# Kernel optimization log

Hardware: AMD Instinct MI355X
Metric: run time of the kernel (lower is better)

Reference implementation:

```python
import jax, jax.numpy as jnp
import numpy as np

B, N, FH, H, FO = 8, 1024, 128, 8, 64
FIN = 2 * FH  # f_hid * 2
NEG = -1e9
SLOPE = 0.2  # leaky_relu negative slope (GAT default)


def setup_inputs() -> dict:
    key = jax.random.key(0)
    ks = jax.random.split(key, 10)
    x = jax.random.normal(ks[0], (B, FIN), jnp.float32)
    A = jax.random.randint(ks[1], (B, N, N), 0, 2, jnp.int32)  # 0/1 dense adjacency
    mask_zero = jnp.ones((B, N, 1), jnp.float32)  # node validity mask
    p_atten = jax.random.uniform(ks[2], (B, N), jnp.float32)  # unused in forward body
    e_atten = jax.random.uniform(ks[3], (B, N, FIN), jnp.float32)
    Npost = jax.random.normal(ks[4], (N, FIN), jnp.float32) * np.float32(1.0 / np.sqrt(FIN))  # kaiming-ish
    w = jax.random.normal(ks[5], (H, FIN, FO), jnp.float32) * np.float32(1.0 / np.sqrt(FIN))
    a_src = jax.random.normal(ks[6], (H, FO), jnp.float32) * np.float32(0.1)
    a_dst = jax.random.normal(ks[7], (H, FO), jnp.float32) * np.float32(0.1)
    bias = jnp.zeros((FO,), jnp.float32)
    return {"x": x, "A": A, "mask_zero": mask_zero, "p_atten": p_atten,
            "e_atten": e_atten, "Npost": Npost, "w": w, "a_src": a_src,
            "a_dst": a_dst, "bias": bias}


def reference(x, A, mask_zero, p_atten, e_atten, Npost, w, a_src, a_dst, bias):
    # broadcast-mul feature gating: x [B,FIN] repeated over N posts, gated by Npost*e_atten
    recx = x[:, None, :] * (Npost[None, :, :] * e_atten)          # [B,N,FIN]
    # BatchGAT (DeepInf-style multi-head graph attention, dropout disabled / eval mode)
    h = jnp.einsum('bnf,hfo->bhno', recx, w)                      # [B,H,N,FO]
    s = jnp.einsum('bhno,ho->bhn', h, a_src)                      # src attention term
    d = jnp.einsum('bhno,ho->bhn', h, a_dst)                      # dst attention term
    logits = jax.nn.leaky_relu(s[:, :, :, None] + d[:, :, None, :], SLOPE)  # [B,H,N,N]
    adj = (A > 0)[:, None, :, :]                                  # [B,1,N,N]
    logits = jnp.where(adj, logits, NEG)
    attn = jax.nn.softmax(logits, axis=-1)                        # masked row softmax
    out = jnp.einsum('bhnm,bhmo->bhno', attn, h) + bias           # aggregate neighbors
    out = out.mean(axis=1)                                        # average heads -> [B,N,FO]
    return out * mask_zero                                        # zero padded nodes
```

## Files before the change

### kernel.cpp

```cpp
#include <hip/hip_runtime.h>

typedef __attribute__((ext_vector_type(8))) short          bf16x8;
typedef __attribute__((ext_vector_type(8))) unsigned short u16x8;
typedef __attribute__((ext_vector_type(4))) unsigned short u16x4;
typedef __attribute__((ext_vector_type(4))) float          f32x4;
typedef __attribute__((ext_vector_type(4))) unsigned int   u32x4;

union U8 { u16x8 u; bf16x8 b; u32x4 w; };
union U4 { u16x4 u; unsigned w[2]; };

__device__ __forceinline__ unsigned short f2bf(float f){
  unsigned u = __float_as_uint(f);
  return (unsigned short)((u + 0x7fffu + ((u >> 16) & 1u)) >> 16);
}
__device__ __forceinline__ unsigned pack_bf16(float lo, float hi){
  unsigned a = __float_as_uint(hi) + 0x8000u;
  unsigned b = __float_as_uint(lo) + 0x8000u;
  return __builtin_amdgcn_perm(a, b, 0x07060302u);
}
__device__ __forceinline__ unsigned maskpack(float e0, float e1, unsigned m){
  unsigned r;
  asm("v_cvt_pk_bf16_f32 %0, %1, %2" : "=v"(r) : "v"(e0), "v"(e1));
  return r & m;
}

#define NN  1024
#define FIN 256
#define NH  8
#define FO  64

__global__ __launch_bounds__(256) void stage0(
    const float* __restrict__ w, const int* __restrict__ A,
    const float* __restrict__ bias, const float* __restrict__ mz,
    unsigned short* __restrict__ wfrag, unsigned* __restrict__ emask,
    float* __restrict__ out)
{
  const int tid = blockIdx.x * 256 + threadIdx.x;
  if (tid < 16384){
    const int lane = tid & 63, ss = (tid >> 6) & 3, kc = (tid >> 8) & 7, h = tid >> 11;
    const int o = 16 * ss + (lane & 15);
    const int f = kc * 32 + (lane >> 4) * 8;
    u16x8 r;
    #pragma unroll
    for (int j = 0; j < 8; j++) r[j] = f2bf(w[(h * FIN + f + j) * FO + o]);
    *(u16x8*)(wfrag + tid * 8) = r;
  }
  #pragma unroll
  for (int k = 0; k < 2; k++){
    const int i = tid + k * 262144;
    out[i] = bias[i & 63] * mz[i >> 6];
  }
  const int4* A4 = (const int4*)A;
  for (int i = tid; i < 1048576; i += 262144){
    const int4 a0 = A4[2 * i], a1 = A4[2 * i + 1];
    u32x4 m;
    m[0] = (a0.x > 0 ? 0xFFFFu : 0u) | (a0.y > 0 ? 0xFFFF0000u : 0u);
    m[1] = (a0.z > 0 ? 0xFFFFu : 0u) | (a0.w > 0 ? 0xFFFF0000u : 0u);
    m[2] = (a1.x > 0 ? 0xFFFFu : 0u) | (a1.y > 0 ? 0xFFFF0000u : 0u);
    m[3] = (a1.z > 0 ? 0xFFFFu : 0u) | (a1.w > 0 ? 0xFFFF0000u : 0u);
    *(u32x4*)(emask + 4 * i) = m;
  }
}

__global__ __launch_bounds__(512, 4) void stageA(
    const float* __restrict__ x, const float* __restrict__ e_at,
    const float* __restrict__ Np, const unsigned short* __restrict__ wfrag,
    const float* __restrict__ a_src, const float* __restrict__ a_dst,
    unsigned short* __restrict__ hT,
    float* __restrict__ Rt, float* __restrict__ expd, float* __restrict__ expd2)
{
  __shared__ unsigned short rex[16 * 264];
  const int t = threadIdx.x;
  const int n0 = blockIdx.x * 16, b = blockIdx.y;

  {
    const int row = t >> 5, f0 = (t & 31) * 8;
    const int nrow = n0 + row;
    const float* ep = e_at + (b * NN + nrow) * FIN + f0;
    const float* qp = Np + nrow * FIN + f0;
    const float* xp = x + b * FIN + f0;
    f32x4 e0 = *(const f32x4*)ep, e1 = *(const f32x4*)(ep + 4);
    f32x4 q0 = *(const f32x4*)qp, q1 = *(const f32x4*)(qp + 4);
    f32x4 x0 = *(const f32x4*)xp, x1 = *(const f32x4*)(xp + 4);
    u16x8 r;
    #pragma unroll
    for (int j = 0; j < 4; j++){
      r[j]     = f2bf(e0[j] * q0[j] * x0[j]);
      r[j + 4] = f2bf(e1[j] * q1[j] * x1[j]);
    }
    *(u16x8*)(rex + row * 264 + f0) = r;
  }
  __syncthreads();

  const int h = t >> 6, lane = t & 63, quad = lane >> 4, l15 = lane & 15;
  const unsigned short* wf = wfrag + h * 16384 + lane * 8;

  f32x4 acc[4] = {};
  #pragma unroll
  for (int kc = 0; kc < 8; kc++){
    U8 a0, bf[4];
    a0.u = *(const u16x8*)(rex + l15 * 264 + kc * 32 + quad * 8);
    #pragma unroll
    for (int ss = 0; ss < 4; ss++) bf[ss].u = *(const u16x8*)(wf + (kc * 4 + ss) * 512);
    #pragma unroll
    for (int ss = 0; ss < 4; ss++)
      acc[ss] = __builtin_amdgcn_mfma_f32_16x16x32_bf16(a0.b, bf[ss].b, acc[ss], 0, 0, 0);
  }

  {
    const int mtile = blockIdx.x >> 1, moff = (blockIdx.x & 1) * 16;
    unsigned short* pan = hT + (size_t)(((b * NH + h) * 32 + mtile) * 64) * 32;
    #pragma unroll
    for (int ss = 0; ss < 4; ss++){
      U4 v;
      v.w[0] = pack_bf16(acc[ss][0], acc[ss][1]);
      v.w[1] = pack_bf16(acc[ss][2], acc[ss][3]);
      *(u16x4*)(pan + (16 * ss + l15) * 32 + moff + quad * 4) = v.u;
    }
  }

  float as4[4], ad4[4];
  #pragma unroll
  for (int ss = 0; ss < 4; ss++){
    as4[ss] = a_src[h * FO + 16 * ss + l15];
    ad4[ss] = a_dst[h * FO + 16 * ss + l15];
  }
  #pragma unroll
  for (int i = 0; i < 4; i++){
    float ps = 0.f, pd = 0.f;
    #pragma unroll
    for (int ss = 0; ss < 4; ss++){ ps += acc[ss][i] * as4[ss]; pd += acc[ss][i] * ad4[ss]; }
    #pragma unroll
    for (int off = 1; off < 16; off <<= 1){
      ps += __shfl_xor(ps, off);
      pd += __shfl_xor(pd, off);
    }
    if (l15 == 0){
      const int idx = (b * NH + h) * NN + n0 + quad * 4 + i;
      Rt[idx]    = __expf(0.8f * ps);
      expd[idx]  = __expf(pd);
      expd2[idx] = __expf(0.2f * pd);
    }
  }
}

__global__ __launch_bounds__(512, 8) void stageB(
    const unsigned* __restrict__ emask,
    const unsigned short* __restrict__ hT,
    const float* __restrict__ Rt,
    const float* __restrict__ expd, const float* __restrict__ expd2,
    const float* __restrict__ mz, float* __restrict__ out)
{
  __shared__ float ed_l[2 * NN];
  __shared__ float e2_l[2 * NN];
  __shared__ float l_l[4 * 16];
  const int t = threadIdx.x;
  const int n0 = blockIdx.x * 32, hq = blockIdx.y, b = blockIdx.z;
  const int w = t >> 6, lane = t & 63, quad = lane >> 4, l15 = lane & 15;
  const int hl = w & 1, rg = (w >> 1) & 1, mh = w >> 2;
  const int h = hq * 2 + hl;

  if (t < 64) l_l[t] = 0.f;
  {
    const float* s1 = expd  + (b * NH + hq * 2) * NN;
    const float* s2 = expd2 + (b * NH + hq * 2) * NN;
    *(f32x4*)(ed_l + t * 4) = *(const f32x4*)(s1 + t * 4);
    *(f32x4*)(e2_l + t * 4) = *(const f32x4*)(s2 + t * 4);
  }
  __syncthreads();

  const int row = n0 + rg * 16 + l15;
  const float Rv = Rt[(b * NH + h) * NN + row];
  const unsigned short* pb = hT + (size_t)(b * NH + h) * 65536 + l15 * 32 + quad * 8;
  const float* edh = ed_l + hl * NN + quad * 8;
  const float* e2h = e2_l + hl * NN + quad * 8;
  const unsigned* emp = emask + ((size_t)(b * NN) + row) * 512 + quad * 4;
  const int c0 = mh * 16;

  U8 pan[4];
  #pragma unroll
  for (int ss = 0; ss < 4; ss++)
    pan[ss].u = *(const u16x8*)(pb + (size_t)c0 * 2048 + ss * 512);
  u32x4 em = *(const u32x4*)(emp + c0 * 16);

  U8 ones;
  #pragma unroll
  for (int j = 0; j < 8; j++) ones.u[j] = 0x3F80;

  f32x4 acc[4] = {};
  f32x4 accl = {};

  for (int cc = 0; cc < 16; cc++){
    const int c = c0 + cc;
    f32x4 d01 = *(const f32x4*)(edh + c * 32);
    f32x4 d23 = *(const f32x4*)(edh + c * 32 + 4);
    f32x4 g01 = *(const f32x4*)(e2h + c * 32);
    f32x4 g23 = *(const f32x4*)(e2h + c * 32 + 4);
    f32x4 p01 = Rv * d01, p23 = Rv * d23;
    U8 p;
    p.w[0] = maskpack(fmaxf(p01[0], g01[0]), fmaxf(p01[1], g01[1]), em[0]);
    p.w[1] = maskpack(fmaxf(p01[2], g01[2]), fmaxf(p01[3], g01[3]), em[1]);
    p.w[2] = maskpack(fmaxf(p23[0], g23[0]), fmaxf(p23[1], g23[1]), em[2]);
    p.w[3] = maskpack(fmaxf(p23[2], g23[2]), fmaxf(p23[3], g23[3]), em[3]);
    #pragma unroll
    for (int ss = 0; ss < 4; ss++)
      acc[ss] = __builtin_amdgcn_mfma_f32_16x16x32_bf16(p.b, pan[ss].b, acc[ss], 0, 0, 0);
    accl = __builtin_amdgcn_mfma_f32_16x16x32_bf16(p.b, ones.b, accl, 0, 0, 0);
    if (cc + 1 < 16){
      #pragma unroll
      for (int ss = 0; ss < 4; ss++)
        pan[ss].u = *(const u16x8*)(pb + (size_t)(c + 1) * 2048 + ss * 512);
      em = *(const u32x4*)(emp + (c + 1) * 16);
    }
  }

  if (l15 == 0){
    #pragma unroll
    for (int i = 0; i < 4; i++)
      atomicAdd(&l_l[(w & 3) * 16 + quad * 4 + i], accl[i]);
  }
  __syncthreads();

  const float* mzp = mz + b * NN + n0 + rg * 16;
  #pragma unroll
  for (int i = 0; i < 4; i++){
    const int r = quad * 4 + i;
    const float invm = (0.125f / l_l[(w & 3) * 16 + r]) * mzp[r];
    float* op = out + (size_t)(b * NN + n0 + rg * 16 + r) * FO + l15;
    #pragma unroll
    for (int ss = 0; ss < 4; ss++)
      atomicAdd(op + ss * 16, acc[ss][i] * invm);
  }
}

extern "C" void kernel_launch(void* const* d_in, const int* in_sizes, int n_in,
                              void* d_out, int out_size, void* d_ws, size_t ws_size,
                              hipStream_t stream)
{
  (void)in_sizes; (void)n_in; (void)out_size; (void)ws_size;
  const float* x    = (const float*)d_in[0];
  const int*   A    = (const int*)d_in[1];
  const float* mz   = (const float*)d_in[2];
  const float* e_at = (const float*)d_in[4];
  const float* Np   = (const float*)d_in[5];
  const float* w    = (const float*)d_in[6];
  const float* asrc = (const float*)d_in[7];
  const float* adst = (const float*)d_in[8];
  const float* bias = (const float*)d_in[9];
  float* out = (float*)d_out;

  char* ws = (char*)d_ws;
  unsigned short* wfrag = (unsigned short*)ws;
  unsigned short* hT    = (unsigned short*)(ws + 262144);
  float* Rt    = (float*)(ws + 8650752);
  float* expd  = (float*)(ws + 8912896);
  float* expd2 = (float*)(ws + 9175040);
  unsigned* emask = (unsigned*)(ws + 9437184);

  stage0<<<dim3(1024), dim3(256), 0, stream>>>(w, A, bias, mz, wfrag, emask, out);
  stageA<<<dim3(64, 8), dim3(512), 0, stream>>>(x, e_at, Np, wfrag, asrc, adst,
                                                hT, Rt, expd, expd2);
  stageB<<<dim3(32, 4, 8), dim3(512), 0, stream>>>(emask, hT, Rt, expd, expd2,
                                                   mz, out);
}
```

Before: 178.7 us.

## Pack adjacency into bitmask and have each stageB wave process two row groups

stage0 now compresses the int adjacency into a 1-bit-per-edge mask with wave ballots, replacing the 16-bit-per-edge mask. This shrinks the mask written to the workspace and read back by stageB by a factor of 16. stageB loads its 32 rows of bits into LDS and expands them through a 16-entry lookup table. Each wave now computes both 16-row groups, so every hT panel fragment loaded from global memory feeds twice as many MFMAs. The launch becomes 256-thread blocks on a 1D grid with a remapped block order. The cost is more registers per thread, extra LDS lookups, and fewer waves per block.

```diff
diff --git a/kernel.cpp b/kernel.cpp
--- a/kernel.cpp
+++ b/kernel.cpp
@@ -32,7 +32,7 @@
 __global__ __launch_bounds__(256) void stage0(
     const float* __restrict__ w, const int* __restrict__ A,
     const float* __restrict__ bias, const float* __restrict__ mz,
-    unsigned short* __restrict__ wfrag, unsigned* __restrict__ emask,
+    unsigned short* __restrict__ wfrag, unsigned long long* __restrict__ Abits,
     float* __restrict__ out)
 {
   const int tid = blockIdx.x * 256 + threadIdx.x;
@@ -50,15 +50,9 @@
     const int i = tid + k * 262144;
     out[i] = bias[i & 63] * mz[i >> 6];
   }
-  const int4* A4 = (const int4*)A;
-  for (int i = tid; i < 1048576; i += 262144){
-    const int4 a0 = A4[2 * i], a1 = A4[2 * i + 1];
-    u32x4 m;
-    m[0] = (a0.x > 0 ? 0xFFFFu : 0u) | (a0.y > 0 ? 0xFFFF0000u : 0u);
-    m[1] = (a0.z > 0 ? 0xFFFFu : 0u) | (a0.w > 0 ? 0xFFFF0000u : 0u);
-    m[2] = (a1.x > 0 ? 0xFFFFu : 0u) | (a1.y > 0 ? 0xFFFF0000u : 0u);
-    m[3] = (a1.z > 0 ? 0xFFFFu : 0u) | (a1.w > 0 ? 0xFFFF0000u : 0u);
-    *(u32x4*)(emask + 4 * i) = m;
+  for (int i = tid; i < 8388608; i += 262144){
+    unsigned long long m = __ballot(A[i] > 0);
+    if ((threadIdx.x & 63) == 0) Abits[i >> 6] = m;
   }
 }
 
@@ -144,8 +138,8 @@
   }
 }
 
-__global__ __launch_bounds__(512, 8) void stageB(
-    const unsigned* __restrict__ emask,
+__global__ __launch_bounds__(256, 4) void stageB(
+    const unsigned* __restrict__ Aw,
     const unsigned short* __restrict__ hT,
     const float* __restrict__ Rt,
     const float* __restrict__ expd, const float* __restrict__ expd2,
@@ -153,83 +147,131 @@
 {
   __shared__ float ed_l[2 * NN];
   __shared__ float e2_l[2 * NN];
+  __shared__ unsigned mask_l[32 * 33];
+  __shared__ __align__(8) unsigned lut[16][2];
   __shared__ float l_l[4 * 16];
+
+  const int fid = blockIdx.x;
+  const int gb = (fid & 7) * 128 + (fid >> 3);
+  const int n0 = (gb & 31) * 32, hq = (gb >> 5) & 3, b = gb >> 7;
+
   const int t = threadIdx.x;
-  const int n0 = blockIdx.x * 32, hq = blockIdx.y, b = blockIdx.z;
   const int w = t >> 6, lane = t & 63, quad = lane >> 4, l15 = lane & 15;
-  const int hl = w & 1, rg = (w >> 1) & 1, mh = w >> 2;
+  const int hl = w & 1, mh = w >> 1;
   const int h = hq * 2 + hl;
 
   if (t < 64) l_l[t] = 0.f;
+  if (t < 16){
+    lut[t][0] = (t & 1 ? 0xFFFFu : 0u) | (t & 2 ? 0xFFFF0000u : 0u);
+    lut[t][1] = (t & 4 ? 0xFFFFu : 0u) | (t & 8 ? 0xFFFF0000u : 0u);
+  }
   {
     const float* s1 = expd  + (b * NH + hq * 2) * NN;
     const float* s2 = expd2 + (b * NH + hq * 2) * NN;
-    *(f32x4*)(ed_l + t * 4) = *(const f32x4*)(s1 + t * 4);
-    *(f32x4*)(e2_l + t * 4) = *(const f32x4*)(s2 + t * 4);
+    *(f32x4*)(ed_l + t * 8)     = *(const f32x4*)(s1 + t * 8);
+    *(f32x4*)(ed_l + t * 8 + 4) = *(const f32x4*)(s1 + t * 8 + 4);
+    *(f32x4*)(e2_l + t * 8)     = *(const f32x4*)(s2 + t * 8);
+    *(f32x4*)(e2_l + t * 8 + 4) = *(const f32x4*)(s2 + t * 8 + 4);
+  }
+  #pragma unroll
+  for (int k = 0; k < 4; k++){
+    const int i = t + k * 256;
+    mask_l[(i >> 5) * 33 + (i & 31)] = Aw[(b * NN + n0 + (i >> 5)) * 32 + (i & 31)];
   }
   __syncthreads();
 
-  const int row = n0 + rg * 16 + l15;
-  const float Rv = Rt[(b * NH + h) * NN + row];
+  const int hb = (b * NH + h) * NN;
+  const float Rv0 = Rt[hb + n0 + l15];
+  const float Rv1 = Rt[hb + n0 + 16 + l15];
   const unsigned short* pb = hT + (size_t)(b * NH + h) * 65536 + l15 * 32 + quad * 8;
   const float* edh = ed_l + hl * NN + quad * 8;
   const float* e2h = e2_l + hl * NN + quad * 8;
-  const unsigned* emp = emask + ((size_t)(b * NN) + row) * 512 + quad * 4;
   const int c0 = mh * 16;
+  const int qs = quad * 8;
 
   U8 pan[4];
   #pragma unroll
   for (int ss = 0; ss < 4; ss++)
     pan[ss].u = *(const u16x8*)(pb + (size_t)c0 * 2048 + ss * 512);
-  u32x4 em = *(const u32x4*)(emp + c0 * 16);
+  unsigned mw0 = mask_l[l15 * 33 + c0];
+  unsigned mw1 = mask_l[(16 + l15) * 33 + c0];
 
   U8 ones;
   #pragma unroll
   for (int j = 0; j < 8; j++) ones.u[j] = 0x3F80;
 
-  f32x4 acc[4] = {};
-  f32x4 accl = {};
+  f32x4 acc0[4] = {}, acc1[4] = {};
+  f32x4 accl0 = {}, accl1 = {};
 
   for (int cc = 0; cc < 16; cc++){
     const int c = c0 + cc;
-    f32x4 d01 = *(const f32x4*)(edh + c * 32);
-    f32x4 d23 = *(const f32x4*)(edh + c * 32 + 4);
-    f32x4 g01 = *(const f32x4*)(e2h + c * 32);
-    f32x4 g23 = *(const f32x4*)(e2h + c * 32 + 4);
-    f32x4 p01 = Rv * d01, p23 = Rv * d23;
-    U8 p;
-    p.w[0] = maskpack(fmaxf(p01[0], g01[0]), fmaxf(p01[1], g01[1]), em[0]);
-    p.w[1] = maskpack(fmaxf(p01[2], g01[2]), fmaxf(p01[3], g01[3]), em[1]);
-    p.w[2] = maskpack(fmaxf(p23[0], g23[0]), fmaxf(p23[1], g23[1]), em[2]);
-    p.w[3] = maskpack(fmaxf(p23[2], g23[2]), fmaxf(p23[3], g23[3]), em[3]);
-    #pragma unroll
-    for (int ss = 0; ss < 4; ss++)
-      acc[ss] = __builtin_amdgcn_mfma_f32_16x16x32_bf16(p.b, pan[ss].b, acc[ss], 0, 0, 0);
-    accl = __builtin_amdgcn_mfma_f32_16x16x32_bf16(p.b, ones.b, accl, 0, 0, 0);
+    const unsigned am0 = (mw0 >> qs) & 0xFF;
+    const unsigned am1 = (mw1 >> qs) & 0xFF;
+    const uint2 la0 = *(const uint2*)&lut[am0 & 15][0];
+    const uint2 lb0 = *(const uint2*)&lut[(am0 >> 4) & 15][0];
+    const uint2 la1 = *(const uint2*)&lut[am1 & 15][0];
+    const uint2 lb1 = *(const uint2*)&lut[(am1 >> 4) & 15][0];
+    if (cc + 1 < 16){
+      mw0 = mask_l[l15 * 33 + c + 1];
+      mw1 = mask_l[(16 + l15) * 33 + c + 1];
+    }
+    const f32x4 d01 = *(const f32x4*)(edh + c * 32);
+    const f32x4 d23 = *(const f32x4*)(edh + c * 32 + 4);
+    const f32x4 g01 = *(const f32x4*)(e2h + c * 32);
+    const f32x4 g23 = *(const f32x4*)(e2h + c * 32 + 4);
+    {
+      const f32x4 p01 = Rv0 * d01, p23 = Rv0 * d23;
+      U8 p;
+      p.w[0] = maskpack(fmaxf(p01[0], g01[0]), fmaxf(p01[1], g01[1]), la0.x);
+      p.w[1] = maskpack(fmaxf(p01[2], g01[2]), fmaxf(p01[3], g01[3]), la0.y);
+      p.w[2] = maskpack(fmaxf(p23[0], g23[0]), fmaxf(p23[1], g23[1]), lb0.x);
+      p.w[3] = maskpack(fmaxf(p23[2], g23[2]), fmaxf(p23[3], g23[3]), lb0.y);
+      #pragma unroll
+      for (int ss = 0; ss < 4; ss++)
+        acc0[ss] = __builtin_amdgcn_mfma_f32_16x16x32_bf16(p.b, pan[ss].b, acc0[ss], 0, 0, 0);
+      accl0 = __builtin_amdgcn_mfma_f32_16x16x32_bf16(p.b, ones.b, accl0, 0, 0, 0);
+    }
+    {
+      const f32x4 p01 = Rv1 * d01, p23 = Rv1 * d23;
+      U8 p;
+      p.w[0] = maskpack(fmaxf(p01[0], g01[0]), fmaxf(p01[1], g01[1]), la1.x);
+      p.w[1] = maskpack(fmaxf(p01[2], g01[2]), fmaxf(p01[3], g01[3]), la1.y);
+      p.w[2] = maskpack(fmaxf(p23[0], g23[0]), fmaxf(p23[1], g23[1]), lb1.x);
+      p.w[3] = maskpack(fmaxf(p23[2], g23[2]), fmaxf(p23[3], g23[3]), lb1.y);
+      #pragma unroll
+      for (int ss = 0; ss < 4; ss++)
+        acc1[ss] = __builtin_amdgcn_mfma_f32_16x16x32_bf16(p.b, pan[ss].b, acc1[ss], 0, 0, 0);
+      accl1 = __builtin_amdgcn_mfma_f32_16x16x32_bf16(p.b, ones.b, accl1, 0, 0, 0);
+    }
     if (cc + 1 < 16){
       #pragma unroll
       for (int ss = 0; ss < 4; ss++)
         pan[ss].u = *(const u16x8*)(pb + (size_t)(c + 1) * 2048 + ss * 512);
-      em = *(const u32x4*)(emp + (c + 1) * 16);
     }
   }
 
   if (l15 == 0){
     #pragma unroll
-    for (int i = 0; i < 4; i++)
-      atomicAdd(&l_l[(w & 3) * 16 + quad * 4 + i], accl[i]);
+    for (int i = 0; i < 4; i++){
+      atomicAdd(&l_l[(hl * 2 + 0) * 16 + quad * 4 + i], accl0[i]);
+      atomicAdd(&l_l[(hl * 2 + 1) * 16 + quad * 4 + i], accl1[i]);
+    }
   }
   __syncthreads();
 
-  const float* mzp = mz + b * NN + n0 + rg * 16;
+  const float* mzp = mz + b * NN + n0;
   #pragma unroll
   for (int i = 0; i < 4; i++){
-    const int r = quad * 4 + i;
-    const float invm = (0.125f / l_l[(w & 3) * 16 + r]) * mzp[r];
-    float* op = out + (size_t)(b * NN + n0 + rg * 16 + r) * FO + l15;
-    #pragma unroll
-    for (int ss = 0; ss < 4; ss++)
-      atomicAdd(op + ss * 16, acc[ss][i] * invm);
+    const int r16 = quad * 4 + i;
+    const float invm0 = (0.125f / l_l[(hl * 2 + 0) * 16 + r16]) * mzp[r16];
+    const float invm1 = (0.125f / l_l[(hl * 2 + 1) * 16 + r16]) * mzp[16 + r16];
+    float* op0 = out + (size_t)(b * NN + n0 + r16) * FO + l15;
+    float* op1 = out + (size_t)(b * NN + n0 + 16 + r16) * FO + l15;
+    #pragma unroll
+    for (int ss = 0; ss < 4; ss++){
+      atomicAdd(op0 + ss * 16, acc0[ss][i] * invm0);
+      atomicAdd(op1 + ss * 16, acc1[ss][i] * invm1);
+    }
   }
 }
 
@@ -255,11 +297,11 @@
   float* Rt    = (float*)(ws + 8650752);
   float* expd  = (float*)(ws + 8912896);
   float* expd2 = (float*)(ws + 9175040);
-  unsigned* emask = (unsigned*)(ws + 9437184);
-
-  stage0<<<dim3(1024), dim3(256), 0, stream>>>(w, A, bias, mz, wfrag, emask, out);
+  unsigned long long* Abits = (unsigned long long*)(ws + 9437184);
+
+  stage0<<<dim3(1024), dim3(256), 0, stream>>>(w, A, bias, mz, wfrag, Abits, out);
   stageA<<<dim3(64, 8), dim3(512), 0, stream>>>(x, e_at, Np, wfrag, asrc, adst,
                                                 hT, Rt, expd, expd2);
-  stageB<<<dim3(32, 4, 8), dim3(512), 0, stream>>>(emask, hT, Rt, expd, expd2,
-                                                   mz, out);
-}
+  stageB<<<dim3(1024), dim3(256), 0, stream>>>((const unsigned*)Abits, hT,
+                                               Rt, expd, expd2, mz, out);
+}
```

Result: faster. 158.0 us (-11.6%).

## Pack adjacency into bitmask in stageA and reduce heads in LDS without atomics

Applied to the files above, without the earlier changes.

The adjacency conversion moves from stage0 into stageA. It now writes 1 bit per edge using wave ballots instead of a 16-bit mask per edge, which shrinks the mask the attention kernel has to read by a large factor. The attention kernel is restructured so that one block handles all 8 heads for a 16-row tile. Head averaging, bias and the node mask are applied through an LDS reduction, replacing global float atomics and the separate output init. Each wave now walks the full 1024 columns with double-buffered panel loads. This cuts parallelism per block and adds bit-expansion ALU work in the inner loop.

```diff
diff --git a/kernel.cpp b/kernel.cpp
--- a/kernel.cpp
+++ b/kernel.cpp
@@ -23,6 +23,11 @@
   asm("v_cvt_pk_bf16_f32 %0, %1, %2" : "=v"(r) : "v"(e0), "v"(e1));
   return r & m;
 }
+__device__ __forceinline__ unsigned bit2half(unsigned m, unsigned off){
+  unsigned lo = __builtin_amdgcn_sbfe((int)m, off, 1u);
+  unsigned hi = __builtin_amdgcn_sbfe((int)m, off + 1u, 1u);
+  return __builtin_amdgcn_perm(hi, lo, 0x05040100u);
+}
 
 #define NN  1024
 #define FIN 256
@@ -30,48 +35,31 @@
 #define FO  64
 
 __global__ __launch_bounds__(256) void stage0(
-    const float* __restrict__ w, const int* __restrict__ A,
-    const float* __restrict__ bias, const float* __restrict__ mz,
-    unsigned short* __restrict__ wfrag, unsigned* __restrict__ emask,
-    float* __restrict__ out)
+    const float* __restrict__ w, unsigned short* __restrict__ wfrag)
 {
   const int tid = blockIdx.x * 256 + threadIdx.x;
-  if (tid < 16384){
-    const int lane = tid & 63, ss = (tid >> 6) & 3, kc = (tid >> 8) & 7, h = tid >> 11;
-    const int o = 16 * ss + (lane & 15);
-    const int f = kc * 32 + (lane >> 4) * 8;
-    u16x8 r;
-    #pragma unroll
-    for (int j = 0; j < 8; j++) r[j] = f2bf(w[(h * FIN + f + j) * FO + o]);
-    *(u16x8*)(wfrag + tid * 8) = r;
-  }
-  #pragma unroll
-  for (int k = 0; k < 2; k++){
-    const int i = tid + k * 262144;
-    out[i] = bias[i & 63] * mz[i >> 6];
-  }
-  const int4* A4 = (const int4*)A;
-  for (int i = tid; i < 1048576; i += 262144){
-    const int4 a0 = A4[2 * i], a1 = A4[2 * i + 1];
-    u32x4 m;
-    m[0] = (a0.x > 0 ? 0xFFFFu : 0u) | (a0.y > 0 ? 0xFFFF0000u : 0u);
-    m[1] = (a0.z > 0 ? 0xFFFFu : 0u) | (a0.w > 0 ? 0xFFFF0000u : 0u);
-    m[2] = (a1.x > 0 ? 0xFFFFu : 0u) | (a1.y > 0 ? 0xFFFF0000u : 0u);
-    m[3] = (a1.z > 0 ? 0xFFFFu : 0u) | (a1.w > 0 ? 0xFFFF0000u : 0u);
-    *(u32x4*)(emask + 4 * i) = m;
-  }
+  const int lane = tid & 63, ss = (tid >> 6) & 3, kc = (tid >> 8) & 7, h = tid >> 11;
+  const int o = 16 * ss + (lane & 15);
+  const int f = kc * 32 + (lane >> 4) * 8;
+  u16x8 r;
+  #pragma unroll
+  for (int j = 0; j < 8; j++) r[j] = f2bf(w[(h * FIN + f + j) * FO + o]);
+  *(u16x8*)(wfrag + tid * 8) = r;
 }
 
 __global__ __launch_bounds__(512, 4) void stageA(
     const float* __restrict__ x, const float* __restrict__ e_at,
     const float* __restrict__ Np, const unsigned short* __restrict__ wfrag,
     const float* __restrict__ a_src, const float* __restrict__ a_dst,
+    const int* __restrict__ A, unsigned long long* __restrict__ Abits,
     unsigned short* __restrict__ hT,
     float* __restrict__ Rt, float* __restrict__ expd, float* __restrict__ expd2)
 {
   __shared__ unsigned short rex[16 * 264];
   const int t = threadIdx.x;
-  const int n0 = blockIdx.x * 16, b = blockIdx.y;
+  const int fid = blockIdx.x;
+  const int b = fid & 7, tile = fid >> 3;
+  const int n0 = tile * 16;
 
   {
     const int row = t >> 5, f0 = (t & 31) * 8;
@@ -108,7 +96,7 @@
   }
 
   {
-    const int mtile = blockIdx.x >> 1, moff = (blockIdx.x & 1) * 16;
+    const int mtile = tile >> 1, moff = (tile & 1) * 16;
     unsigned short* pan = hT + (size_t)(((b * NH + h) * 32 + mtile) * 64) * 32;
     #pragma unroll
     for (int ss = 0; ss < 4; ss++){
@@ -142,46 +130,56 @@
       expd2[idx] = __expf(0.2f * pd);
     }
   }
-}
-
-__global__ __launch_bounds__(512, 8) void stageB(
-    const unsigned* __restrict__ emask,
+
+  {
+    const int seg = b * 1048576 + tile * 16384;
+    #pragma unroll 4
+    for (int k = 0; k < 32; k++){
+      const int i = seg + k * 512 + t;
+      unsigned long long m = __ballot(A[i] > 0);
+      if ((t & 63) == 0) Abits[i >> 6] = m;
+    }
+  }
+}
+
+__global__ __launch_bounds__(512, 4) void attnBC(
+    const unsigned* __restrict__ Aw,
     const unsigned short* __restrict__ hT,
     const float* __restrict__ Rt,
     const float* __restrict__ expd, const float* __restrict__ expd2,
-    const float* __restrict__ mz, float* __restrict__ out)
-{
-  __shared__ float ed_l[2 * NN];
-  __shared__ float e2_l[2 * NN];
-  __shared__ float l_l[4 * 16];
+    const float* __restrict__ bias, const float* __restrict__ mz,
+    float* __restrict__ out)
+{
+  __shared__ float smem[16384];
+
+  const int fid = blockIdx.x;
+  const int b = fid & 7, rt = fid >> 3;
+  const int n0 = rt * 16;
+
   const int t = threadIdx.x;
-  const int n0 = blockIdx.x * 32, hq = blockIdx.y, b = blockIdx.z;
-  const int w = t >> 6, lane = t & 63, quad = lane >> 4, l15 = lane & 15;
-  const int hl = w & 1, rg = (w >> 1) & 1, mh = w >> 2;
-  const int h = hq * 2 + hl;
-
-  if (t < 64) l_l[t] = 0.f;
-  {
-    const float* s1 = expd  + (b * NH + hq * 2) * NN;
-    const float* s2 = expd2 + (b * NH + hq * 2) * NN;
-    *(f32x4*)(ed_l + t * 4) = *(const f32x4*)(s1 + t * 4);
-    *(f32x4*)(e2_l + t * 4) = *(const f32x4*)(s2 + t * 4);
-  }
-  __syncthreads();
-
-  const int row = n0 + rg * 16 + l15;
-  const float Rv = Rt[(b * NH + h) * NN + row];
+  const int h = t >> 6, lane = t & 63, quad = lane >> 4, l15 = lane & 15;
+
+  #pragma unroll
+  for (int k = 0; k < 4; k++){
+    *(f32x4*)(smem + k * 2048 + t * 4) =
+        *(const f32x4*)(expd + b * 8192 + k * 2048 + t * 4);
+    *(f32x4*)(smem + 8192 + k * 2048 + t * 4) =
+        *(const f32x4*)(expd2 + b * 8192 + k * 2048 + t * 4);
+  }
+  __syncthreads();
+
+  const float Rv = Rt[(b * NH + h) * NN + n0 + l15];
   const unsigned short* pb = hT + (size_t)(b * NH + h) * 65536 + l15 * 32 + quad * 8;
-  const float* edh = ed_l + hl * NN + quad * 8;
-  const float* e2h = e2_l + hl * NN + quad * 8;
-  const unsigned* emp = emask + ((size_t)(b * NN) + row) * 512 + quad * 4;
-  const int c0 = mh * 16;
-
-  U8 pan[4];
+  const float* edh = smem + h * 1024 + quad * 8;
+  const float* e2h = smem + 8192 + h * 1024 + quad * 8;
+  const unsigned* awp = Aw + (b * NN + n0) * 32;
+  const unsigned qs = (unsigned)(quad * 8);
+
+  U8 panc[4], pann[4];
   #pragma unroll
   for (int ss = 0; ss < 4; ss++)
-    pan[ss].u = *(const u16x8*)(pb + (size_t)c0 * 2048 + ss * 512);
-  u32x4 em = *(const u32x4*)(emp + c0 * 16);
+    panc[ss].u = *(const u16x8*)(pb + ss * 512);
+  unsigned mwc = awp[l15 * 32], mwn;
 
   U8 ones;
   #pragma unroll
@@ -190,46 +188,58 @@
   f32x4 acc[4] = {};
   f32x4 accl = {};
 
-  for (int cc = 0; cc < 16; cc++){
-    const int c = c0 + cc;
-    f32x4 d01 = *(const f32x4*)(edh + c * 32);
-    f32x4 d23 = *(const f32x4*)(edh + c * 32 + 4);
-    f32x4 g01 = *(const f32x4*)(e2h + c * 32);
-    f32x4 g23 = *(const f32x4*)(e2h + c * 32 + 4);
-    f32x4 p01 = Rv * d01, p23 = Rv * d23;
-    U8 p;
-    p.w[0] = maskpack(fmaxf(p01[0], g01[0]), fmaxf(p01[1], g01[1]), em[0]);
-    p.w[1] = maskpack(fmaxf(p01[2], g01[2]), fmaxf(p01[3], g01[3]), em[1]);
-    p.w[2] = maskpack(fmaxf(p23[0], g23[0]), fmaxf(p23[1], g23[1]), em[2]);
-    p.w[3] = maskpack(fmaxf(p23[2], g23[2]), fmaxf(p23[3], g23[3]), em[3]);
-    #pragma unroll
-    for (int ss = 0; ss < 4; ss++)
-      acc[ss] = __builtin_amdgcn_mfma_f32_16x16x32_bf16(p.b, pan[ss].b, acc[ss], 0, 0, 0);
-    accl = __builtin_amdgcn_mfma_f32_16x16x32_bf16(p.b, ones.b, accl, 0, 0, 0);
-    if (cc + 1 < 16){
+  #pragma unroll
+  for (int c = 0; c < 32; c++){
+    if (c + 1 < 32){
       #pragma unroll
       for (int ss = 0; ss < 4; ss++)
-        pan[ss].u = *(const u16x8*)(pb + (size_t)(c + 1) * 2048 + ss * 512);
-      em = *(const u32x4*)(emp + (c + 1) * 16);
-    }
-  }
-
-  if (l15 == 0){
-    #pragma unroll
-    for (int i = 0; i < 4; i++)
-      atomicAdd(&l_l[(w & 3) * 16 + quad * 4 + i], accl[i]);
-  }
-  __syncthreads();
-
-  const float* mzp = mz + b * NN + n0 + rg * 16;
+        pann[ss].u = *(const u16x8*)(pb + (size_t)(c + 1) * 2048 + ss * 512);
+      mwn = awp[l15 * 32 + c + 1];
+    }
+    const unsigned lax = bit2half(mwc, qs + 0u), lay = bit2half(mwc, qs + 2u);
+    const unsigned lbx = bit2half(mwc, qs + 4u), lby = bit2half(mwc, qs + 6u);
+    const f32x4 d01 = *(const f32x4*)(edh + c * 32);
+    const f32x4 d23 = *(const f32x4*)(edh + c * 32 + 4);
+    const f32x4 g01 = *(const f32x4*)(e2h + c * 32);
+    const f32x4 g23 = *(const f32x4*)(e2h + c * 32 + 4);
+    const f32x4 p01 = Rv * d01, p23 = Rv * d23;
+    U8 p;
+    p.w[0] = maskpack(fmaxf(p01[0], g01[0]), fmaxf(p01[1], g01[1]), lax);
+    p.w[1] = maskpack(fmaxf(p01[2], g01[2]), fmaxf(p01[3], g01[3]), lay);
+    p.w[2] = maskpack(fmaxf(p23[0], g23[0]), fmaxf(p23[1], g23[1]), lbx);
+    p.w[3] = maskpack(fmaxf(p23[2], g23[2]), fmaxf(p23[3], g23[3]), lby);
+    #pragma unroll
+    for (int ss = 0; ss < 4; ss++)
+      acc[ss] = __builtin_amdgcn_mfma_f32_16x16x32_bf16(p.b, panc[ss].b, acc[ss], 0, 0, 0);
+    accl = __builtin_amdgcn_mfma_f32_16x16x32_bf16(p.b, ones.b, accl, 0, 0, 0);
+    if (c + 1 < 32){
+      #pragma unroll
+      for (int ss = 0; ss < 4; ss++) panc[ss] = pann[ss];
+      mwc = mwn;
+    }
+  }
+
+  __syncthreads();
+
+  float* buf = smem;
   #pragma unroll
   for (int i = 0; i < 4; i++){
-    const int r = quad * 4 + i;
-    const float invm = (0.125f / l_l[(w & 3) * 16 + r]) * mzp[r];
-    float* op = out + (size_t)(b * NN + n0 + rg * 16 + r) * FO + l15;
+    const float inv = 1.0f / accl[i];
     #pragma unroll
     for (int ss = 0; ss < 4; ss++)
-      atomicAdd(op + ss * 16, acc[ss][i] * invm);
+      buf[h * 1040 + (quad * 4 + i) * 65 + ss * 16 + l15] = acc[ss][i] * inv;
+  }
+  __syncthreads();
+
+  #pragma unroll
+  for (int k = 0; k < 2; k++){
+    const int e = k * 512 + t;
+    const int row = e >> 6, col = e & 63;
+    float s = 0.f;
+    #pragma unroll
+    for (int hh = 0; hh < NH; hh++) s += buf[hh * 1040 + row * 65 + col];
+    out[(size_t)(b * NN + n0 + row) * FO + col] =
+        (0.125f * s + bias[col]) * mz[b * NN + n0 + row];
   }
 }
 
@@ -255,11 +265,11 @@
   float* Rt    = (float*)(ws + 8650752);
   float* expd  = (float*)(ws + 8912896);
   float* expd2 = (float*)(ws + 9175040);
-  unsigned* emask = (unsigned*)(ws + 9437184);
-
-  stage0<<<dim3(1024), dim3(256), 0, stream>>>(w, A, bias, mz, wfrag, emask, out);
-  stageA<<<dim3(64, 8), dim3(512), 0, stream>>>(x, e_at, Np, wfrag, asrc, adst,
-                                                hT, Rt, expd, expd2);
-  stageB<<<dim3(32, 4, 8), dim3(512), 0, stream>>>(emask, hT, Rt, expd, expd2,
-                                                   mz, out);
-}
+  unsigned long long* Abits = (unsigned long long*)(ws + 9437184);
+
+  stage0<<<dim3(64), dim3(256), 0, stream>>>(w, wfrag);
+  stageA<<<dim3(512), dim3(512), 0, stream>>>(x, e_at, Np, wfrag, asrc, adst,
+                                              A, Abits, hT, Rt, expd, expd2);
+  attnBC<<<dim3(512), dim3(512), 0, stream>>>((const unsigned*)Abits, hT,
+                                              Rt, expd, expd2, bias, mz, out);
+}
```

New measurement: 151.0 us. 1.18x faster.
